# Performance work log

Measured on AMD Instinct MI355X. Metric: run time of the kernel, lower is better.

The kernel has to match this reference:

```python
import jax, jax.numpy as jnp
import numpy as np
import math

B, S, E, H, DK = 2, 2048, 1024, 16, 64  # batch, seq, embed, heads, d_k (= n_wires)

def setup_inputs() -> dict:
    key = jax.random.key(0)
    k1, k2, k3, k4, k5 = jax.random.split(key, 5)
    scale = 0.02
    return {
        "x": jax.random.normal(k1, (B, S, E), dtype=jnp.float32),
        "Wk": jax.random.normal(k2, (E, E), dtype=jnp.float32) * scale,
        "Wv": jax.random.normal(k3, (E, E), dtype=jnp.float32) * scale,
        "Wq": jax.random.normal(k4, (H, DK, E), dtype=jnp.float32) * scale,
        "theta": jax.random.normal(k5, (DK,), dtype=jnp.float32) * scale,
    }

def reference(x, Wk, Wv, Wq, theta):
    batch, seq, embed = x.shape
    n_heads, d_k = Wq.shape[0], Wq.shape[1]
    # K, V projections (nn.Linear, no bias): x @ W.T
    k = (x @ Wk.T).reshape(batch, seq, n_heads, d_k).transpose(0, 2, 1, 3)  # [B,H,S,dk]
    v = (x @ Wv.T).reshape(batch, seq, n_heads, d_k).transpose(0, 2, 1, 3)  # [B,H,S,dk]
    # Quantum query path: per-head linear proj -> RX(proj_i) then RX(theta_i) on wire i from |0>,
    # MeasureAll(PauliZ) on independent wires gives <Z_i> = cos(proj_i + theta_i) exactly.
    proj = jnp.einsum('bse,hde->bhsd', x, Wq)          # [B,H,S,dk]
    q = jnp.cos(proj + theta)                           # [B,H,S,dk]
    scores = jnp.einsum('bhsd,bhtd->bhst', q, k) / math.sqrt(d_k)  # [B,H,S,S]
    attn = jax.nn.softmax(scores, axis=-1)
    out = jnp.einsum('bhst,bhtd->bhsd', attn, v)        # [B,H,S,dk]
    return out.transpose(0, 2, 1, 3).reshape(batch, seq, embed)
```

## Files before the change

kernel.cpp:

```cpp
#include <hip/hip_runtime.h>
#include <hip/hip_bf16.h>

constexpr int B  = 2;
constexpr int S  = 2048;
constexpr int E  = 1024;
constexpr int H  = 16;
constexpr int DK = 64;
constexpr int M  = B * S;
constexpr int N3 = 3 * E;
constexpr long RSZ = (long)B * H * S * DK;

using bf16x8 = __attribute__((ext_vector_type(8))) __bf16;
using bf16x4 = __attribute__((ext_vector_type(4))) __bf16;
using f32x4  = __attribute__((ext_vector_type(4))) float;

__device__ __forceinline__ void async16(__bf16* lds, const __bf16* g) {
    __builtin_amdgcn_global_load_lds(
        (const __attribute__((address_space(1))) void*)g,
        (__attribute__((address_space(3))) void*)lds, 16, 0, 0);
}

__global__ __launch_bounds__(256)
void cvt_kernel(const float* __restrict__ x, const float* __restrict__ Wk,
                const float* __restrict__ Wv, const float* __restrict__ Wq,
                __bf16* __restrict__ xb, __bf16* __restrict__ wall) {
    const long e = ((long)blockIdx.x * 256 + threadIdx.x) * 4;
    const float* src;
    __bf16* dst;
    if (e < (long)M * E) { src = x + e; dst = xb + e; }
    else {
        const long e2 = e - (long)M * E;
        const int which = (int)(e2 >> 20);
        const long off  = e2 & ((1L << 20) - 1);
        src = (which == 0 ? Wk : which == 1 ? Wv : Wq) + off;
        dst = wall + e2;
    }
    float4 f = *reinterpret_cast<const float4*>(src);
    bf16x4 o;
    o[0] = (__bf16)f.x; o[1] = (__bf16)f.y; o[2] = (__bf16)f.z; o[3] = (__bf16)f.w;
    *reinterpret_cast<bf16x4*>(dst) = o;
}

__global__ __launch_bounds__(256, 2)
void qkv_gemm(const __bf16* __restrict__ xb, const __bf16* __restrict__ wall,
              const float* __restrict__ theta, __bf16* __restrict__ kvq) {
    __shared__ __align__(1024) __bf16 As[128 * 32];
    __shared__ __align__(1024) __bf16 Bs[128 * 32];

    const int t    = threadIdx.x;
    const int lane = t & 63;
    const int w    = t >> 6;
    const int quad = lane >> 4;
    const int l16  = lane & 15;
    const int wm   = w >> 1, wn = w & 1;
    const int mbase = blockIdx.y * 128;
    const int nbase = blockIdx.x * 128;

    f32x4 acc[4][4];
    #pragma unroll
    for (int i = 0; i < 4; i++)
        #pragma unroll
        for (int j = 0; j < 4; j++)
            acc[i][j] = f32x4{0.f, 0.f, 0.f, 0.f};

    const int arow = t >> 2;
    const int achk = t & 3;
    const __bf16* ga = xb   + (long)(mbase + arow) * E + achk * 8;
    const __bf16* gb = wall + (long)(nbase + arow) * E + achk * 8;

    for (int kk = 0; kk < E; kk += 32) {
        __syncthreads();
        #pragma unroll
        for (int c = 0; c < 2; c++) {
            async16(&As[(c * 256 + w * 64) * 8], ga + (long)c * 64 * E + kk);
            async16(&Bs[(c * 256 + w * 64) * 8], gb + (long)c * 64 * E + kk);
        }
        __syncthreads();

        bf16x8 a[4], b[4];
        #pragma unroll
        for (int i = 0; i < 4; i++)
            a[i] = *reinterpret_cast<const bf16x8*>(&As[(wm * 64 + i * 16 + l16) * 32 + quad * 8]);
        #pragma unroll
        for (int j = 0; j < 4; j++)
            b[j] = *reinterpret_cast<const bf16x8*>(&Bs[(wn * 64 + j * 16 + l16) * 32 + quad * 8]);
        #pragma unroll
        for (int i = 0; i < 4; i++)
            #pragma unroll
            for (int j = 0; j < 4; j++)
                acc[i][j] = __builtin_amdgcn_mfma_f32_16x16x32_bf16(a[i], b[j], acc[i][j], 0, 0, 0);
    }

    const int region = nbase >> 10;
    __bf16* dst = kvq + region * RSZ;
    float th[4];
    if (region == 2) {
        #pragma unroll
        for (int j = 0; j < 4; j++) th[j] = theta[j * 16 + l16];
    }
    #pragma unroll
    for (int i = 0; i < 4; i++) {
        const int row0 = mbase + wm * 64 + i * 16 + quad * 4;
        #pragma unroll
        for (int j = 0; j < 4; j++) {
            const int cir = (nbase & 1023) + wn * 64 + j * 16 + l16;
            const int h = cir >> 6, d = cir & 63;
            #pragma unroll
            for (int r = 0; r < 4; r++) {
                const int row = row0 + r;
                const int bb = row >> 11, s = row & 2047;
                float v = acc[i][j][r];
                if (region == 2) v = cosf(v + th[j]) * 0.125f;
                dst[((long)(bb * H + h) * S + s) * DK + d] = (__bf16)v;
            }
        }
    }
}

__global__ __launch_bounds__(256)
void vtrans_kernel(const __bf16* __restrict__ vr, __bf16* __restrict__ vt) {
    __shared__ __bf16 tile[64 * 64];
    const int t = threadIdx.x;
    const int bh = blockIdx.y;
    const int sbase = blockIdx.x * 64;
    const __bf16* src = vr + ((long)bh * S + sbase) * DK;
    #pragma unroll
    for (int rr = 0; rr < 2; rr++) {
        const int idx = rr * 256 + t;
        const int sl = idx >> 3, dc = idx & 7;
        bf16x8 v = *reinterpret_cast<const bf16x8*>(src + sl * DK + dc * 8);
        const int dcs = dc ^ (sl >> 3);
        *reinterpret_cast<bf16x8*>(&tile[sl * 64 + dcs * 8]) = v;
    }
    __syncthreads();
    __bf16* dstp = vt + (long)bh * DK * S + sbase;
    #pragma unroll
    for (int rr = 0; rr < 2; rr++) {
        const int idx = rr * 256 + t;
        const int dl = idx >> 3, sc = idx & 7;
        bf16x8 o;
        #pragma unroll
        for (int j = 0; j < 8; j++) {
            const int srow = sc * 8 + j;
            const int dcs = (dl >> 3) ^ (srow >> 3);
            o[j] = tile[srow * 64 + dcs * 8 + (dl & 7)];
        }
        *reinterpret_cast<bf16x8*>(dstp + (long)dl * S + sc * 8) = o;
    }
}

__global__ __launch_bounds__(256, 2)
void attn_kernel(const __bf16* __restrict__ q_ws, const __bf16* __restrict__ k_ws,
                 const __bf16* __restrict__ v_ws, float* __restrict__ out) {
    __shared__ __align__(1024) __bf16 Ks[2][64 * 64];
    __shared__ __align__(1024) __bf16 Vs[2][64 * 64];
    __shared__ __align__(16)   __bf16 p_lds[4][32][72];

    const int lane = threadIdx.x & 63;
    const int w    = threadIdx.x >> 6;
    const int quad = lane >> 4;
    const int l16  = lane & 15;
    const int bh    = blockIdx.y;
    const int qbase = blockIdx.x * 128 + w * 32;

    const __bf16* qp = q_ws + (long)bh * S * DK;
    const __bf16* kp = k_ws + (long)bh * S * DK;
    const __bf16* vp = v_ws + (long)bh * DK * S;

    const int sr  = lane >> 3;
    const int sc  = lane & 7;
    const int scs = sc ^ sr;

    bf16x8 aq[2][2];
    #pragma unroll
    for (int mt = 0; mt < 2; mt++)
        #pragma unroll
        for (int ks = 0; ks < 2; ks++)
            aq[mt][ks] = *reinterpret_cast<const bf16x8*>(
                qp + (long)(qbase + mt * 16 + l16) * DK + ks * 32 + quad * 8);

    bf16x8 vone;
    #pragma unroll
    for (int j = 0; j < 8; j++) vone[j] = (__bf16)1.0f;

    f32x4 o[2][4];
    #pragma unroll
    for (int i = 0; i < 2; i++)
        #pragma unroll
        for (int j = 0; j < 4; j++) o[i][j] = f32x4{0.f, 0.f, 0.f, 0.f};
    f32x4 ls[2] = {f32x4{0.f, 0.f, 0.f, 0.f}, f32x4{0.f, 0.f, 0.f, 0.f}};

    #pragma unroll
    for (int i = 0; i < 2; i++) {
        const int row = i * 32 + w * 8;
        async16(&Ks[0][row * 64], kp + (long)(row + sr) * DK + scs * 8);
        async16(&Vs[0][row * 64], vp + (long)(row + sr) * S + scs * 8);
    }

    for (int it = 0; it < S / 64; it++) {
        const int cur = it & 1;
        __syncthreads();

        if (it + 1 < S / 64) {
            const int kt1 = (it + 1) * 64;
            #pragma unroll
            for (int i = 0; i < 2; i++) {
                const int row = i * 32 + w * 8;
                async16(&Ks[cur ^ 1][row * 64], kp + (long)(kt1 + row + sr) * DK + scs * 8);
                async16(&Vs[cur ^ 1][row * 64], vp + (long)(row + sr) * S + kt1 + scs * 8);
            }
        }

        f32x4 sacc[2][4];
        #pragma unroll
        for (int i = 0; i < 2; i++)
            #pragma unroll
            for (int j = 0; j < 4; j++) sacc[i][j] = f32x4{0.f, 0.f, 0.f, 0.f};
        #pragma unroll
        for (int ks = 0; ks < 2; ks++) {
            bf16x8 bk[4];
            #pragma unroll
            for (int nt = 0; nt < 4; nt++)
                bk[nt] = *reinterpret_cast<const bf16x8*>(
                    &Ks[cur][(nt * 16 + l16) * 64 + ((ks * 4 + quad) ^ (l16 & 7)) * 8]);
            #pragma unroll
            for (int mt = 0; mt < 2; mt++)
                #pragma unroll
                for (int nt = 0; nt < 4; nt++)
                    sacc[mt][nt] = __builtin_amdgcn_mfma_f32_16x16x32_bf16(
                        aq[mt][ks], bk[nt], sacc[mt][nt], 0, 0, 0);
        }
        #pragma unroll
        for (int mt = 0; mt < 2; mt++)
            #pragma unroll
            for (int r = 0; r < 4; r++)
                #pragma unroll
                for (int nt = 0; nt < 4; nt++)
                    p_lds[w][mt * 16 + quad * 4 + r][nt * 16 + l16] =
                        (__bf16)__expf(sacc[mt][nt][r]);
        #pragma unroll
        for (int ks = 0; ks < 2; ks++) {
            bf16x8 ap[2];
            #pragma unroll
            for (int mt = 0; mt < 2; mt++)
                ap[mt] = *reinterpret_cast<const bf16x8*>(
                    &p_lds[w][mt * 16 + l16][ks * 32 + quad * 8]);
            bf16x8 bv[4];
            #pragma unroll
            for (int nd = 0; nd < 4; nd++)
                bv[nd] = *reinterpret_cast<const bf16x8*>(
                    &Vs[cur][(nd * 16 + l16) * 64 + ((ks * 4 + quad) ^ (l16 & 7)) * 8]);
            #pragma unroll
            for (int mt = 0; mt < 2; mt++) {
                ls[mt] = __builtin_amdgcn_mfma_f32_16x16x32_bf16(ap[mt], vone, ls[mt], 0, 0, 0);
                #pragma unroll
                for (int nd = 0; nd < 4; nd++)
                    o[mt][nd] = __builtin_amdgcn_mfma_f32_16x16x32_bf16(
                        ap[mt], bv[nd], o[mt][nd], 0, 0, 0);
            }
        }
    }

    const int b = bh >> 4, h = bh & 15;
    #pragma unroll
    for (int mt = 0; mt < 2; mt++) {
        #pragma unroll
        for (int r = 0; r < 4; r++) {
            const float inv = 1.0f / ls[mt][r];
            const int srow = qbase + mt * 16 + quad * 4 + r;
            #pragma unroll
            for (int nd = 0; nd < 4; nd++)
                out[(long)(b * S + srow) * E + h * DK + nd * 16 + l16] = o[mt][nd][r] * inv;
        }
    }
}

__device__ inline bf16x8 cvt_frag(const float* __restrict__ p) {
    float4 f0 = *reinterpret_cast<const float4*>(p);
    float4 f1 = *reinterpret_cast<const float4*>(p + 4);
    bf16x8 r;
    r[0] = (__bf16)f0.x; r[1] = (__bf16)f0.y; r[2] = (__bf16)f0.z; r[3] = (__bf16)f0.w;
    r[4] = (__bf16)f1.x; r[5] = (__bf16)f1.y; r[6] = (__bf16)f1.z; r[7] = (__bf16)f1.w;
    return r;
}
template <int MODE>
__global__ __launch_bounds__(256, 2)
void proj_kernel(const float* __restrict__ x, const float* __restrict__ W,
                 const float* __restrict__ theta, __bf16* __restrict__ out) {
    const int lane = threadIdx.x & 63;
    const int w    = threadIdx.x >> 6;
    const int quad = lane >> 4;
    const int l16  = lane & 15;
    const int mbase = blockIdx.y * 128 + w * 32;
    const int nbase = blockIdx.x * 128;
    f32x4 acc[2][8];
    #pragma unroll
    for (int i = 0; i < 2; i++)
        #pragma unroll
        for (int j = 0; j < 8; j++) acc[i][j] = f32x4{0.f, 0.f, 0.f, 0.f};
    float th[4];
    if (MODE == 2) {
        #pragma unroll
        for (int j = 0; j < 4; j++) th[j] = theta[j * 16 + l16];
    }
    for (int kk = 0; kk < E; kk += 32) {
        bf16x8 a[2], b[8];
        #pragma unroll
        for (int mt = 0; mt < 2; mt++)
            a[mt] = cvt_frag(x + (long)(mbase + mt * 16 + l16) * E + kk + quad * 8);
        #pragma unroll
        for (int nt = 0; nt < 8; nt++)
            b[nt] = cvt_frag(W + (long)(nbase + nt * 16 + l16) * E + kk + quad * 8);
        #pragma unroll
        for (int mt = 0; mt < 2; mt++)
            #pragma unroll
            for (int nt = 0; nt < 8; nt++)
                acc[mt][nt] = __builtin_amdgcn_mfma_f32_16x16x32_bf16(a[mt], b[nt], acc[mt][nt], 0, 0, 0);
    }
    #pragma unroll
    for (int mt = 0; mt < 2; mt++) {
        const int row0 = mbase + mt * 16 + quad * 4;
        #pragma unroll
        for (int nt = 0; nt < 8; nt++) {
            const int col = nbase + nt * 16 + l16;
            const int h = col >> 6, d = col & 63;
            #pragma unroll
            for (int r = 0; r < 4; r++) {
                const int row = row0 + r;
                const int bb = row >> 11, s = row & 2047;
                float v = acc[mt][nt][r];
                if (MODE == 2) v = cosf(v + th[nt & 3]) * 0.125f;
                long idx;
                if (MODE == 1) idx = ((long)(bb * H + h) * DK + d) * S + s;
                else           idx = ((long)(bb * H + h) * S + s) * DK + d;
                out[idx] = (__bf16)v;
            }
        }
    }
}

extern "C" void kernel_launch(void* const* d_in, const int* in_sizes, int n_in,
                              void* d_out, int out_size, void* d_ws, size_t ws_size,
                              hipStream_t stream) {
    const float* x     = (const float*)d_in[0];
    const float* Wk    = (const float*)d_in[1];
    const float* Wv    = (const float*)d_in[2];
    const float* Wq    = (const float*)d_in[3];
    const float* theta = (const float*)d_in[4];
    float* out = (float*)d_out;

    __bf16* kvq  = (__bf16*)d_ws;
    __bf16* xb   = kvq + 3 * RSZ;
    __bf16* wall = xb + (long)M * E;
    __bf16* k_ws = kvq;
    __bf16* vrow = kvq + RSZ;
    __bf16* q_ws = kvq + 2 * RSZ;
    __bf16* v_t  = xb;

    const size_t need = (3 * RSZ + (long)M * E + (long)N3 * E) * 2;
    dim3 blk(256);
    if (ws_size >= need) {
        cvt_kernel<<<dim3(7168), blk, 0, stream>>>(x, Wk, Wv, Wq, xb, wall);
        qkv_gemm<<<dim3(N3 / 128, M / 128), blk, 0, stream>>>(xb, wall, theta, kvq);
        vtrans_kernel<<<dim3(S / 64, B * H), blk, 0, stream>>>(vrow, v_t);
    } else {
        v_t = vrow;
        dim3 gp(E / 128, M / 128);
        proj_kernel<0><<<gp, blk, 0, stream>>>(x, Wk, nullptr, k_ws);
        proj_kernel<1><<<gp, blk, 0, stream>>>(x, Wv, nullptr, v_t);
        proj_kernel<2><<<gp, blk, 0, stream>>>(x, Wq, theta, q_ws);
    }

    attn_kernel<<<dim3(S / 128, B * H), blk, 0, stream>>>(q_ws, k_ws, v_t, out);
}
```

Baseline: 190.5 us.

## Double-buffer QKV GEMM, fuse V transpose into its epilogue, swizzle LDS

The QKV GEMM now prefetches the next K-slice into a second LDS buffer while computing the current one, and reads tiles through an XOR swizzle. The V-projection epilogue transposes through LDS and writes V already in d-major layout, so the separate vtrans kernel and its global round trip go away. The attention kernel stores P in an MFMA-fragment-ordered LDS layout to cut bank conflicts, and both kernels request 3 blocks per SM. The trade-offs are more LDS per GEMM block, extra syncs in the V blocks, and register pressure from the higher occupancy hint.

```diff
diff --git a/kernel.cpp b/kernel.cpp
--- a/kernel.cpp
+++ b/kernel.cpp
@@ -41,11 +41,11 @@
     *reinterpret_cast<bf16x4*>(dst) = o;
 }
 
-__global__ __launch_bounds__(256, 2)
+__global__ __launch_bounds__(256, 3)
 void qkv_gemm(const __bf16* __restrict__ xb, const __bf16* __restrict__ wall,
               const float* __restrict__ theta, __bf16* __restrict__ kvq) {
-    __shared__ __align__(1024) __bf16 As[128 * 32];
-    __shared__ __align__(1024) __bf16 Bs[128 * 32];
+    __shared__ __align__(1024) __bf16 smem[4 * 128 * 32];
+    __bf16* tile = smem;
 
     const int t    = threadIdx.x;
     const int lane = t & 63;
@@ -63,27 +63,45 @@
         for (int j = 0; j < 4; j++)
             acc[i][j] = f32x4{0.f, 0.f, 0.f, 0.f};
 
-    const int arow = t >> 2;
-    const int achk = t & 3;
-    const __bf16* ga = xb   + (long)(mbase + arow) * E + achk * 8;
-    const __bf16* gb = wall + (long)(nbase + arow) * E + achk * 8;
-
-    for (int kk = 0; kk < E; kk += 32) {
+    const int srow = lane >> 2;
+    const int srcc = (lane & 3) ^ ((lane >> 3) & 3);
+    const __bf16* ga = xb   + (long)(mbase + srow) * E + srcc * 8;
+    const __bf16* gb = wall + (long)(nbase + srow) * E + srcc * 8;
+
+    const int csw = (l16 >> 1) & 3;
+
+    #pragma unroll
+    for (int c = 0; c < 2; c++) {
+        async16(smem +        (c * 64 + w * 16) * 32, ga + (long)(c * 64 + w * 16) * E);
+        async16(smem + 8192 + (c * 64 + w * 16) * 32, gb + (long)(c * 64 + w * 16) * E);
+    }
+
+    for (int it = 0; it < E / 32; it++) {
+        const int cur = it & 1;
         __syncthreads();
-        #pragma unroll
-        for (int c = 0; c < 2; c++) {
-            async16(&As[(c * 256 + w * 64) * 8], ga + (long)c * 64 * E + kk);
-            async16(&Bs[(c * 256 + w * 64) * 8], gb + (long)c * 64 * E + kk);
-        }
-        __syncthreads();
-
+
+        if (it + 1 < E / 32) {
+            const int kk1 = (it + 1) * 32;
+            #pragma unroll
+            for (int c = 0; c < 2; c++) {
+                async16(smem + (cur ^ 1) * 4096 +        (c * 64 + w * 16) * 32,
+                        ga + (long)(c * 64 + w * 16) * E + kk1);
+                async16(smem + (cur ^ 1) * 4096 + 8192 + (c * 64 + w * 16) * 32,
+                        gb + (long)(c * 64 + w * 16) * E + kk1);
+            }
+        }
+
+        const __bf16* Asb = smem + cur * 4096;
+        const __bf16* Bsb = smem + cur * 4096 + 8192;
         bf16x8 a[4], b[4];
         #pragma unroll
         for (int i = 0; i < 4; i++)
-            a[i] = *reinterpret_cast<const bf16x8*>(&As[(wm * 64 + i * 16 + l16) * 32 + quad * 8]);
+            a[i] = *reinterpret_cast<const bf16x8*>(
+                &Asb[(wm * 64 + i * 16 + l16) * 32 + (quad ^ csw) * 8]);
         #pragma unroll
         for (int j = 0; j < 4; j++)
-            b[j] = *reinterpret_cast<const bf16x8*>(&Bs[(wn * 64 + j * 16 + l16) * 32 + quad * 8]);
+            b[j] = *reinterpret_cast<const bf16x8*>(
+                &Bsb[(wn * 64 + j * 16 + l16) * 32 + (quad ^ csw) * 8]);
         #pragma unroll
         for (int i = 0; i < 4; i++)
             #pragma unroll
@@ -92,69 +110,67 @@
     }
 
     const int region = nbase >> 10;
-    __bf16* dst = kvq + region * RSZ;
-    float th[4];
-    if (region == 2) {
-        #pragma unroll
-        for (int j = 0; j < 4; j++) th[j] = theta[j * 16 + l16];
-    }
-    #pragma unroll
-    for (int i = 0; i < 4; i++) {
-        const int row0 = mbase + wm * 64 + i * 16 + quad * 4;
-        #pragma unroll
-        for (int j = 0; j < 4; j++) {
-            const int cir = (nbase & 1023) + wn * 64 + j * 16 + l16;
-            const int h = cir >> 6, d = cir & 63;
-            #pragma unroll
-            for (int r = 0; r < 4; r++) {
-                const int row = row0 + r;
-                const int bb = row >> 11, s = row & 2047;
-                float v = acc[i][j][r];
-                if (region == 2) v = cosf(v + th[j]) * 0.125f;
-                dst[((long)(bb * H + h) * S + s) * DK + d] = (__bf16)v;
-            }
-        }
-    }
-}
-
-__global__ __launch_bounds__(256)
-void vtrans_kernel(const __bf16* __restrict__ vr, __bf16* __restrict__ vt) {
-    __shared__ __bf16 tile[64 * 64];
-    const int t = threadIdx.x;
-    const int bh = blockIdx.y;
-    const int sbase = blockIdx.x * 64;
-    const __bf16* src = vr + ((long)bh * S + sbase) * DK;
-    #pragma unroll
-    for (int rr = 0; rr < 2; rr++) {
-        const int idx = rr * 256 + t;
-        const int sl = idx >> 3, dc = idx & 7;
-        bf16x8 v = *reinterpret_cast<const bf16x8*>(src + sl * DK + dc * 8);
-        const int dcs = dc ^ (sl >> 3);
-        *reinterpret_cast<bf16x8*>(&tile[sl * 64 + dcs * 8]) = v;
-    }
-    __syncthreads();
-    __bf16* dstp = vt + (long)bh * DK * S + sbase;
-    #pragma unroll
-    for (int rr = 0; rr < 2; rr++) {
-        const int idx = rr * 256 + t;
-        const int dl = idx >> 3, sc = idx & 7;
-        bf16x8 o;
-        #pragma unroll
-        for (int j = 0; j < 8; j++) {
-            const int srow = sc * 8 + j;
-            const int dcs = (dl >> 3) ^ (srow >> 3);
-            o[j] = tile[srow * 64 + dcs * 8 + (dl & 7)];
-        }
-        *reinterpret_cast<bf16x8*>(dstp + (long)dl * S + sc * 8) = o;
-    }
-}
-
-__global__ __launch_bounds__(256, 2)
+    const int bb = mbase >> 11;
+    if (region == 1) {
+        __syncthreads();
+        #pragma unroll
+        for (int i = 0; i < 4; i++) {
+            const int cchunk = wm * 8 + i * 2 + (quad >> 1);
+            #pragma unroll
+            for (int j = 0; j < 4; j++) {
+                const int cirb = wn * 64 + j * 16 + l16;
+                const int cs = cchunk ^ l16;
+                bf16x4 pk;
+                #pragma unroll
+                for (int r = 0; r < 4; r++) pk[r] = (__bf16)acc[i][j][r];
+                *reinterpret_cast<bf16x4*>(&tile[cirb * 128 + cs * 8 + (quad & 1) * 4]) = pk;
+            }
+        }
+        __syncthreads();
+        const int h0 = (nbase & 1023) >> 6;
+        __bf16* vt = kvq + RSZ;
+        #pragma unroll
+        for (int p = 0; p < 8; p++) {
+            const int dcol = p * 16 + (t >> 4);
+            const int lc = t & 15;
+            const int cs2 = lc ^ (dcol & 15);
+            bf16x8 vv = *reinterpret_cast<const bf16x8*>(&tile[dcol * 128 + cs2 * 8]);
+            const int hh = h0 + (dcol >> 6), d = dcol & 63;
+            *reinterpret_cast<bf16x8*>(
+                &vt[((long)(bb * H + hh) * DK + d) * S + (mbase & 2047) + lc * 8]) = vv;
+        }
+    } else {
+        __bf16* dst = kvq + (region == 2 ? 2 * RSZ : 0);
+        float th[4];
+        if (region == 2) {
+            #pragma unroll
+            for (int j = 0; j < 4; j++) th[j] = theta[j * 16 + l16];
+        }
+        #pragma unroll
+        for (int i = 0; i < 4; i++) {
+            const int row0 = mbase + wm * 64 + i * 16 + quad * 4;
+            #pragma unroll
+            for (int j = 0; j < 4; j++) {
+                const int cir = (nbase & 1023) + wn * 64 + j * 16 + l16;
+                const int h = cir >> 6, d = cir & 63;
+                #pragma unroll
+                for (int r = 0; r < 4; r++) {
+                    const int s = (row0 + r) & 2047;
+                    float v = acc[i][j][r];
+                    if (region == 2) v = cosf(v + th[j]) * 0.125f;
+                    dst[((long)(bb * H + h) * S + s) * DK + d] = (__bf16)v;
+                }
+            }
+        }
+    }
+}
+
+__global__ __launch_bounds__(256, 3)
 void attn_kernel(const __bf16* __restrict__ q_ws, const __bf16* __restrict__ k_ws,
                  const __bf16* __restrict__ v_ws, float* __restrict__ out) {
     __shared__ __align__(1024) __bf16 Ks[2][64 * 64];
     __shared__ __align__(1024) __bf16 Vs[2][64 * 64];
-    __shared__ __align__(16)   __bf16 p_lds[4][32][72];
+    __shared__ __align__(16)   __bf16 p_c[4][2048];
 
     const int lane = threadIdx.x & 63;
     const int w    = threadIdx.x >> 6;
@@ -190,6 +206,8 @@
         for (int j = 0; j < 4; j++) o[i][j] = f32x4{0.f, 0.f, 0.f, 0.f};
     f32x4 ls[2] = {f32x4{0.f, 0.f, 0.f, 0.f}, f32x4{0.f, 0.f, 0.f, 0.f}};
 
+    const int prd = (l16 & 3) * 256 + (quad >> 1) * 64 + (l16 >> 2) * 16 + (quad & 1) * 8;
+
     #pragma unroll
     for (int i = 0; i < 2; i++) {
         const int row = i * 32 + w * 8;
@@ -236,7 +254,7 @@
             for (int r = 0; r < 4; r++)
                 #pragma unroll
                 for (int nt = 0; nt < 4; nt++)
-                    p_lds[w][mt * 16 + quad * 4 + r][nt * 16 + l16] =
+                    p_c[w][((mt * 4 + r) * 4 + nt) * 64 + lane] =
                         (__bf16)__expf(sacc[mt][nt][r]);
         #pragma unroll
         for (int ks = 0; ks < 2; ks++) {
@@ -244,7 +262,7 @@
             #pragma unroll
             for (int mt = 0; mt < 2; mt++)
                 ap[mt] = *reinterpret_cast<const bf16x8*>(
-                    &p_lds[w][mt * 16 + l16][ks * 32 + quad * 8]);
+                    &p_c[w][prd + mt * 1024 + ks * 128]);
             bf16x8 bv[4];
             #pragma unroll
             for (int nd = 0; nd < 4; nd++)
@@ -353,18 +371,15 @@
     __bf16* xb   = kvq + 3 * RSZ;
     __bf16* wall = xb + (long)M * E;
     __bf16* k_ws = kvq;
-    __bf16* vrow = kvq + RSZ;
+    __bf16* v_t  = kvq + RSZ;
     __bf16* q_ws = kvq + 2 * RSZ;
-    __bf16* v_t  = xb;
 
     const size_t need = (3 * RSZ + (long)M * E + (long)N3 * E) * 2;
     dim3 blk(256);
     if (ws_size >= need) {
         cvt_kernel<<<dim3(7168), blk, 0, stream>>>(x, Wk, Wv, Wq, xb, wall);
         qkv_gemm<<<dim3(N3 / 128, M / 128), blk, 0, stream>>>(xb, wall, theta, kvq);
-        vtrans_kernel<<<dim3(S / 64, B * H), blk, 0, stream>>>(vrow, v_t);
     } else {
-        v_t = vrow;
         dim3 gp(E / 128, M / 128);
         proj_kernel<0><<<gp, blk, 0, stream>>>(x, Wk, nullptr, k_ws);
         proj_kernel<1><<<gp, blk, 0, stream>>>(x, Wv, nullptr, v_t);
```

After: 186.0 us. 1.02x faster.
